# Kernel optimization log

Hardware: AMD Instinct MI355X
Metric: run time of the kernel (lower is better)

The kernel has to match this reference:

```python
import jax, jax.numpy as jnp
import numpy as np

N_NODES = 100000
D_IN = 128
D_OUT = 128
B, T, S = 8, 4096, 25


def setup_inputs() -> dict:
    key = jax.random.key(0)
    k1, k2, k3 = jax.random.split(key, 3)
    features = jax.random.normal(k1, (N_NODES, D_IN), dtype=jnp.float32)
    sample_res = jax.random.randint(k2, (B, T, S), 0, N_NODES, dtype=jnp.int64)
    # glorot-uniform init for [D_IN, D_OUT]
    limit = np.sqrt(6.0 / (D_IN + D_OUT)).astype(np.float32)
    weights = jax.random.uniform(k3, (D_IN, D_OUT), dtype=jnp.float32,
                                 minval=-limit, maxval=limit)
    return {"features": features, "sample_res": sample_res, "weights": weights}


def reference(features, sample_res, weights):
    # gather neighbor embeddings: [B, T, S, D]
    sampled = features[sample_res]
    # mean over sampled-neighbor axis -> [B, T, D]
    neigh_vecs = jnp.mean(sampled, axis=2)
    # shared linear transform + relu (bias=False per init defaults)
    out = jnp.einsum('btd,do->bto', neigh_vecs, weights)
    return jax.nn.relu(out)
```

## Files before the change

kernel.cpp:

```cpp
#include <hip/hip_runtime.h>


#define DEG 25
#define DIM 128

typedef __attribute__((ext_vector_type(8))) short short8;
typedef __attribute__((ext_vector_type(4))) float floatx4;
typedef __attribute__((ext_vector_type(4))) unsigned int uintx4;

__device__ __forceinline__ unsigned short f2bf(float f) {
    unsigned u = __float_as_uint(f);
    return (unsigned short)((u + 0x7fffu + ((u >> 16) & 1u)) >> 16);
}

#define BSTRIDE 136

__global__ __launch_bounds__(256, 2) void gemm_fw(
    const float* __restrict__ A,
    const float* __restrict__ B,
    unsigned short* __restrict__ G,
    int M)
{
    __shared__ unsigned short sBt[DIM * BSTRIDE];

    const int tid = threadIdx.x;

    {
        const float4* B4 = (const float4*)B;
#pragma unroll
        for (int i = 0; i < 16; ++i) {
            const int linear = i * 256 + tid;
            const int k  = linear >> 5;
            const int c4 = linear & 31;
            const float4 v = B4[linear];
            const int n = c4 * 4;
            sBt[(n + 0) * BSTRIDE + k] = f2bf(v.x);
            sBt[(n + 1) * BSTRIDE + k] = f2bf(v.y);
            sBt[(n + 2) * BSTRIDE + k] = f2bf(v.z);
            sBt[(n + 3) * BSTRIDE + k] = f2bf(v.w);
        }
    }
    __syncthreads();

    const int wave = tid >> 6;
    const int lane = tid & 63;
    const int quad = lane >> 4;
    const int l16  = lane & 15;

    const int rw0 = blockIdx.x * 128 + wave * 32;

    floatx4 acc[2][8];
#pragma unroll
    for (int mt = 0; mt < 2; ++mt)
#pragma unroll
        for (int nt = 0; nt < 8; ++nt)
            acc[mt][nt] = (floatx4){0.f, 0.f, 0.f, 0.f};

#pragma unroll
    for (int kt = 0; kt < 4; ++kt) {
        const int k0 = kt * 32;

        short8 afrag[2];
#pragma unroll
        for (int mt = 0; mt < 2; ++mt) {
            int row = rw0 + mt * 16 + l16;
            if (row >= M) row = M - 1;
            const float* ap = A + (size_t)row * DIM + k0 + quad * 8;
            const float4 x = *(const float4*)ap;
            const float4 y = *(const float4*)(ap + 4);
            unsigned p0 = (unsigned)f2bf(x.x) | ((unsigned)f2bf(x.y) << 16);
            unsigned p1 = (unsigned)f2bf(x.z) | ((unsigned)f2bf(x.w) << 16);
            unsigned p2 = (unsigned)f2bf(y.x) | ((unsigned)f2bf(y.y) << 16);
            unsigned p3 = (unsigned)f2bf(y.z) | ((unsigned)f2bf(y.w) << 16);
            uintx4 packed = (uintx4){p0, p1, p2, p3};
            afrag[mt] = __builtin_bit_cast(short8, packed);
        }

#pragma unroll
        for (int nt = 0; nt < 8; ++nt) {
            const uintx4 u = *(const uintx4*)&sBt[(nt * 16 + l16) * BSTRIDE + k0 + quad * 8];
            const short8 bfrag = __builtin_bit_cast(short8, u);
#pragma unroll
            for (int mt = 0; mt < 2; ++mt)
                acc[mt][nt] = __builtin_amdgcn_mfma_f32_16x16x32_bf16(
                    afrag[mt], bfrag, acc[mt][nt], 0, 0, 0);
        }
    }

    __syncthreads();
    {
        unsigned short* sT = sBt + wave * (32 * BSTRIDE);
#pragma unroll
        for (int mt = 0; mt < 2; ++mt)
#pragma unroll
            for (int nt = 0; nt < 8; ++nt)
#pragma unroll
                for (int r = 0; r < 4; ++r)
                    sT[(mt * 16 + quad * 4 + r) * BSTRIDE + nt * 16 + l16] =
                        f2bf(acc[mt][nt][r]);
    }
    __syncthreads();
    {
        const unsigned short* sT = sBt + wave * (32 * BSTRIDE);
        const int h    = lane & 1;
        const int nrow = lane >> 1;
        const int node = rw0 + nrow;
        if (node < M) {
            uintx4* G4 = (uintx4*)G;
#pragma unroll
            for (int c = 0; c < 8; ++c) {
                const uintx4 u = *(const uintx4*)&sT[nrow * BSTRIDE + c * 16 + h * 8];
                __builtin_nontemporal_store(u, &G4[((size_t)c * M + node) * 2 + h]);
            }
        }
    }
}

#define ROWS_PB 128

__global__ __launch_bounds__(256, 4) void gather_mean_relu_c(
    const unsigned short* __restrict__ G,
    const int* __restrict__ idx,
    float* __restrict__ out,
    int n_rows, int n_nodes)
{
    __shared__ int sIdx[ROWS_PB * DEG];

    const int tid  = threadIdx.x;
    const int c    = blockIdx.x & 7;
    const int rb   = blockIdx.x >> 3;
    const int row0 = rb * ROWS_PB;

    const int* ib = idx + (size_t)row0 * DEG;
    for (int i = tid; i < ROWS_PB * DEG; i += 256)
        sIdx[i] = __builtin_nontemporal_load(ib + i);
    __syncthreads();

    const int h = tid & 1;
    const int r = tid >> 1;
    const uintx4* __restrict__ Gc =
        (const uintx4*)G + (size_t)c * n_nodes * 2 + h;

    float a0 = 0.f, a1 = 0.f, a2 = 0.f, a3 = 0.f;
    float a4 = 0.f, a5 = 0.f, a6 = 0.f, a7 = 0.f;
    const int* ip = &sIdx[r * DEG];

#pragma unroll
    for (int sb = 0; sb < 5; ++sb) {
        uintx4 v[5];
#pragma unroll
        for (int s = 0; s < 5; ++s)
            v[s] = Gc[(size_t)(unsigned)ip[sb * 5 + s] * 2];
#pragma unroll
        for (int s = 0; s < 5; ++s) {
            a0 += __uint_as_float(v[s].x << 16);
            a1 += __uint_as_float(v[s].x & 0xffff0000u);
            a2 += __uint_as_float(v[s].y << 16);
            a3 += __uint_as_float(v[s].y & 0xffff0000u);
            a4 += __uint_as_float(v[s].z << 16);
            a5 += __uint_as_float(v[s].z & 0xffff0000u);
            a6 += __uint_as_float(v[s].w << 16);
            a7 += __uint_as_float(v[s].w & 0xffff0000u);
        }
    }

    const float inv = 1.0f / 25.0f;
    const floatx4 o0 = (floatx4){fmaxf(a0 * inv, 0.f), fmaxf(a1 * inv, 0.f),
                                 fmaxf(a2 * inv, 0.f), fmaxf(a3 * inv, 0.f)};
    const floatx4 o1 = (floatx4){fmaxf(a4 * inv, 0.f), fmaxf(a5 * inv, 0.f),
                                 fmaxf(a6 * inv, 0.f), fmaxf(a7 * inv, 0.f)};
    floatx4* op = (floatx4*)(out + (size_t)(row0 + r) * DIM + c * 16 + h * 8);
    __builtin_nontemporal_store(o0, op);
    __builtin_nontemporal_store(o1, op + 1);
}

#define RPB 16
#define CG 32

__device__ __forceinline__ float4 relu4(float4 v) {
    return make_float4(fmaxf(v.x, 0.f), fmaxf(v.y, 0.f),
                       fmaxf(v.z, 0.f), fmaxf(v.w, 0.f));
}

__global__ __launch_bounds__(256, 4) void gcn_fused(
    const float* __restrict__ F, const int* __restrict__ idx,
    const float* __restrict__ W, float* __restrict__ out, int n_rows)
{
    __shared__ float4 sV[RPB * CG];
    __shared__ int    sIdx[RPB * DEG];

    const float4* F4 = (const float4*)F;
    const float4* W4 = (const float4*)W;
    float4* out4 = (float4*)out;

    const int tid = threadIdx.x;
    const int row0 = blockIdx.x * RPB;

    for (int i = tid; i < RPB * DEG; i += 256)
        sIdx[i] = idx[(size_t)row0 * DEG + i];
    __syncthreads();

    const int cg = tid & 31;
    const int rs = tid >> 5;

#pragma unroll
    for (int rr = 0; rr < 2; ++rr) {
        const int r = rs + rr * 8;
        int j[DEG];
#pragma unroll
        for (int s = 0; s < DEG; ++s) j[s] = sIdx[r * DEG + s];
        float4 acc = make_float4(0.f, 0.f, 0.f, 0.f);
#pragma unroll
        for (int s = 0; s < DEG; ++s) {
            float4 f = F4[(size_t)j[s] * CG + cg];
            acc.x += f.x; acc.y += f.y; acc.z += f.z; acc.w += f.w;
        }
        const float inv = 1.0f / 25.0f;
        acc.x *= inv; acc.y *= inv; acc.z *= inv; acc.w *= inv;
        sV[r * CG + cg] = acc;
    }
    __syncthreads();

    const float4* vA = &sV[rs * CG];
    const float4* vB = &sV[(rs + 8) * CG];
    float4 o0 = make_float4(0.f, 0.f, 0.f, 0.f);
    float4 o1 = make_float4(0.f, 0.f, 0.f, 0.f);
#pragma unroll 4
    for (int d4 = 0; d4 < CG; ++d4) {
        const float4 a = vA[d4];
        const float4 b = vB[d4];
        const float4 w0 = W4[(size_t)(4 * d4 + 0) * CG + cg];
        const float4 w1 = W4[(size_t)(4 * d4 + 1) * CG + cg];
        const float4 w2 = W4[(size_t)(4 * d4 + 2) * CG + cg];
        const float4 w3 = W4[(size_t)(4 * d4 + 3) * CG + cg];
        o0.x += a.x*w0.x + a.y*w1.x + a.z*w2.x + a.w*w3.x;
        o0.y += a.x*w0.y + a.y*w1.y + a.z*w2.y + a.w*w3.y;
        o0.z += a.x*w0.z + a.y*w1.z + a.z*w2.z + a.w*w3.z;
        o0.w += a.x*w0.w + a.y*w1.w + a.z*w2.w + a.w*w3.w;
        o1.x += b.x*w0.x + b.y*w1.x + b.z*w2.x + b.w*w3.x;
        o1.y += b.x*w0.y + b.y*w1.y + b.z*w2.y + b.w*w3.y;
        o1.z += b.x*w0.z + b.y*w1.z + b.z*w2.z + b.w*w3.z;
        o1.w += b.x*w0.w + b.y*w1.w + b.z*w2.w + b.w*w3.w;
    }
    out4[(size_t)(row0 + rs) * CG + cg]     = relu4(o0);
    out4[(size_t)(row0 + rs + 8) * CG + cg] = relu4(o1);
}

extern "C" void kernel_launch(void* const* d_in, const int* in_sizes, int n_in,
                              void* d_out, int out_size, void* d_ws, size_t ws_size,
                              hipStream_t stream) {
    const float* F   = (const float*)d_in[0];
    const int*   idx = (const int*)d_in[1];
    const float* W   = (const float*)d_in[2];
    float* out = (float*)d_out;

    const int n_nodes = in_sizes[0] / DIM;
    const int n_rows  = in_sizes[1] / DEG;

    const size_t need = (size_t)n_nodes * DIM * sizeof(unsigned short);
    if (ws_size >= need && (n_rows & (ROWS_PB - 1)) == 0) {
        unsigned short* G = (unsigned short*)d_ws;
        gemm_fw<<<(n_nodes + 127) / 128, 256, 0, stream>>>(F, W, G, n_nodes);
        gather_mean_relu_c<<<(n_rows / ROWS_PB) * 8, 256, 0, stream>>>(
            G, idx, out, n_rows, n_nodes);
    } else {
        gcn_fused<<<n_rows / RPB, 256, 0, stream>>>(F, idx, W, out, n_rows);
    }
}
```

Measured before the change: 143.3 us.

## Partition node table into cache-sized slices and gather per slice with reduction pass

Splits the projected bf16 node table into four 25000-node partitions, each stored as two 64-column halves with a zero pad row. The gather kernel now filters every row's neighbor indices to one partition so each block's working set fits in cache, and writes fp32 partial sums to a workspace. A new reduce kernel adds the four partition partials and applies mean and ReLU. This trades extra partial-sum traffic and an extra launch for better gather locality, and the fast path is hardwired to exactly 100000 nodes.

```diff
diff --git a/kernel.cpp b/kernel.cpp
--- a/kernel.cpp
+++ b/kernel.cpp
@@ -3,6 +3,8 @@
 
 #define DEG 25
 #define DIM 128
+#define NPP 25000
+#define NPP1 25001
 
 typedef __attribute__((ext_vector_type(8))) short short8;
 typedef __attribute__((ext_vector_type(4))) float floatx4;
@@ -102,76 +104,135 @@
     __syncthreads();
     {
         const unsigned short* sT = sBt + wave * (32 * BSTRIDE);
-        const int h    = lane & 1;
-        const int nrow = lane >> 1;
-        const int node = rw0 + nrow;
-        if (node < M) {
-            uintx4* G4 = (uintx4*)G;
-#pragma unroll
-            for (int c = 0; c < 8; ++c) {
-                const uintx4 u = *(const uintx4*)&sT[nrow * BSTRIDE + c * 16 + h * 8];
-                __builtin_nontemporal_store(u, &G4[((size_t)c * M + node) * 2 + h]);
+        const int oct   = lane & 7;
+        const int nrow8 = lane >> 3;
+        uintx4* G4 = (uintx4*)G;
+#pragma unroll
+        for (int g = 0; g < 4; ++g) {
+            const int lrow = g * 8 + nrow8;
+            const int node = rw0 + lrow;
+            if (node < M) {
+                const unsigned p     = (unsigned)node / NPP;
+                const unsigned local = (unsigned)node - p * NPP;
+#pragma unroll
+                for (int h = 0; h < 2; ++h) {
+                    const uintx4 u = *(const uintx4*)
+                        &sT[lrow * BSTRIDE + h * 64 + oct * 8];
+                    __builtin_nontemporal_store(u,
+                        &G4[((size_t)(p * 2 + h) * NPP1 + local) * 8 + oct]);
+                }
             }
         }
-    }
-}
-
-#define ROWS_PB 128
-
-__global__ __launch_bounds__(256, 4) void gather_mean_relu_c(
+        if (blockIdx.x == 0 && tid < 64) {
+            const int sl = tid >> 3, o = tid & 7;
+            __builtin_nontemporal_store((uintx4){0, 0, 0, 0},
+                &G4[((size_t)sl * NPP1 + NPP) * 8 + o]);
+        }
+    }
+}
+
+#define GRB 128
+
+__global__ __launch_bounds__(256, 4) void gather_partial(
     const unsigned short* __restrict__ G,
     const int* __restrict__ idx,
-    float* __restrict__ out,
-    int n_rows, int n_nodes)
+    float* __restrict__ P,
+    int n_rows)
 {
-    __shared__ int sIdx[ROWS_PB * DEG];
+    __shared__ int sIdx[GRB * DEG];
+    __shared__ int sCnt[GRB];
 
     const int tid  = threadIdx.x;
     const int c    = blockIdx.x & 7;
+    const int p    = c >> 1;
     const int rb   = blockIdx.x >> 3;
-    const int row0 = rb * ROWS_PB;
+    const int row0 = rb * GRB;
+    const int lo   = p * NPP;
 
     const int* ib = idx + (size_t)row0 * DEG;
-    for (int i = tid; i < ROWS_PB * DEG; i += 256)
+    for (int i = tid; i < GRB * DEG; i += 256)
         sIdx[i] = __builtin_nontemporal_load(ib + i);
     __syncthreads();
 
-    const int h = tid & 1;
-    const int r = tid >> 1;
+    if (tid < GRB) {
+        int* lp = &sIdx[tid * DEG];
+        int cnt = 0;
+#pragma unroll
+        for (int s = 0; s < DEG; ++s) {
+            const unsigned d = (unsigned)(lp[s] - lo);
+            if (d < NPP) lp[cnt++] = (int)d;
+        }
+        const int m = ((cnt + 4) / 5) * 5;
+        for (int i = cnt; i < m; ++i) lp[i] = NPP;
+        sCnt[tid] = m;
+    }
+    __syncthreads();
+
+    const int oct = tid & 7;
+    const int rg  = tid >> 3;
     const uintx4* __restrict__ Gc =
-        (const uintx4*)G + (size_t)c * n_nodes * 2 + h;
-
-    float a0 = 0.f, a1 = 0.f, a2 = 0.f, a3 = 0.f;
-    float a4 = 0.f, a5 = 0.f, a6 = 0.f, a7 = 0.f;
-    const int* ip = &sIdx[r * DEG];
-
-#pragma unroll
-    for (int sb = 0; sb < 5; ++sb) {
-        uintx4 v[5];
-#pragma unroll
-        for (int s = 0; s < 5; ++s)
-            v[s] = Gc[(size_t)(unsigned)ip[sb * 5 + s] * 2];
-#pragma unroll
-        for (int s = 0; s < 5; ++s) {
-            a0 += __uint_as_float(v[s].x << 16);
-            a1 += __uint_as_float(v[s].x & 0xffff0000u);
-            a2 += __uint_as_float(v[s].y << 16);
-            a3 += __uint_as_float(v[s].y & 0xffff0000u);
-            a4 += __uint_as_float(v[s].z << 16);
-            a5 += __uint_as_float(v[s].z & 0xffff0000u);
-            a6 += __uint_as_float(v[s].w << 16);
-            a7 += __uint_as_float(v[s].w & 0xffff0000u);
-        }
-    }
-
+        (const uintx4*)G + (size_t)c * NPP1 * 8 + oct;
+
+#pragma unroll
+    for (int rr = 0; rr < 4; ++rr) {
+        const int r = rr * 32 + rg;
+        const int m = sCnt[r];
+        const int* lp = &sIdx[r * DEG];
+
+        float a0 = 0.f, a1 = 0.f, a2 = 0.f, a3 = 0.f;
+        float a4 = 0.f, a5 = 0.f, a6 = 0.f, a7 = 0.f;
+
+        for (int i = 0; i < m; i += 5) {
+            const uintx4 v0 = Gc[(size_t)lp[i + 0] * 8];
+            const uintx4 v1 = Gc[(size_t)lp[i + 1] * 8];
+            const uintx4 v2 = Gc[(size_t)lp[i + 2] * 8];
+            const uintx4 v3 = Gc[(size_t)lp[i + 3] * 8];
+            const uintx4 v4 = Gc[(size_t)lp[i + 4] * 8];
+#pragma unroll
+            for (int k = 0; k < 5; ++k) {
+                const uintx4 v = (k == 0) ? v0 : (k == 1) ? v1 :
+                                 (k == 2) ? v2 : (k == 3) ? v3 : v4;
+                a0 += __uint_as_float(v.x << 16);
+                a1 += __uint_as_float(v.x & 0xffff0000u);
+                a2 += __uint_as_float(v.y << 16);
+                a3 += __uint_as_float(v.y & 0xffff0000u);
+                a4 += __uint_as_float(v.z << 16);
+                a5 += __uint_as_float(v.z & 0xffff0000u);
+                a6 += __uint_as_float(v.w << 16);
+                a7 += __uint_as_float(v.w & 0xffff0000u);
+            }
+        }
+
+        floatx4* Pp = (floatx4*)P + ((size_t)c * n_rows + row0 + r) * 16 + oct * 2;
+        __builtin_nontemporal_store((floatx4){a0, a1, a2, a3}, Pp);
+        __builtin_nontemporal_store((floatx4){a4, a5, a6, a7}, Pp + 1);
+    }
+}
+
+__global__ __launch_bounds__(256, 4) void reduce_relu(
+    const float* __restrict__ P, float* __restrict__ out, int n_rows)
+{
+    const int total = n_rows * 32;
+    const floatx4* P4 = (const floatx4*)P;
+    floatx4* o4 = (floatx4*)out;
     const float inv = 1.0f / 25.0f;
-    const floatx4 o0 = (floatx4){fmaxf(a0 * inv, 0.f), fmaxf(a1 * inv, 0.f),
-                                 fmaxf(a2 * inv, 0.f), fmaxf(a3 * inv, 0.f)};
-    const floatx4 o1 = (floatx4){fmaxf(a4 * inv, 0.f), fmaxf(a5 * inv, 0.f),
-                                 fmaxf(a6 * inv, 0.f), fmaxf(a7 * inv, 0.f)};
-    floatx4* op = (floatx4*)(out + (size_t)(row0 + r) * DIM + c * 16 + h * 8);
-    __builtin_nontemporal_store(o0, op);
-    __builtin_nontemporal_store(o1, op + 1);
+    const size_t sl = (size_t)n_rows * 16;
+
+    for (int i = blockIdx.x * 256 + threadIdx.x; i < total;
+         i += gridDim.x * 256) {
+        const int r   = i >> 5;
+        const int rem = i & 31;
+        const int h   = rem >> 4;
+        const int j4  = rem & 15;
+        const size_t rbase = (size_t)r * 16 + j4;
+        floatx4 s = __builtin_nontemporal_load(&P4[(size_t)(0 + h) * sl + rbase]);
+        s = s + __builtin_nontemporal_load(&P4[(size_t)(2 + h) * sl + rbase]);
+        s = s + __builtin_nontemporal_load(&P4[(size_t)(4 + h) * sl + rbase]);
+        s = s + __builtin_nontemporal_load(&P4[(size_t)(6 + h) * sl + rbase]);
+        const floatx4 o = {fmaxf(s.x * inv, 0.f), fmaxf(s.y * inv, 0.f),
+                           fmaxf(s.z * inv, 0.f), fmaxf(s.w * inv, 0.f)};
+        __builtin_nontemporal_store(o, &o4[(size_t)r * 32 + rem]);
+    }
 }
 
 #define RPB 16
@@ -257,12 +318,16 @@
     const int n_nodes = in_sizes[0] / DIM;
     const int n_rows  = in_sizes[1] / DEG;
 
-    const size_t need = (size_t)n_nodes * DIM * sizeof(unsigned short);
-    if (ws_size >= need && (n_rows & (ROWS_PB - 1)) == 0) {
+    const size_t gbytes = (size_t)8 * NPP1 * 64 * sizeof(unsigned short);
+    const size_t poff   = (gbytes + 1023) & ~(size_t)1023;
+    const size_t need   = poff + (size_t)8 * n_rows * 64 * sizeof(float);
+
+    if (n_nodes == 100000 && ws_size >= need && (n_rows & (GRB - 1)) == 0) {
         unsigned short* G = (unsigned short*)d_ws;
+        float* P = (float*)((char*)d_ws + poff);
         gemm_fw<<<(n_nodes + 127) / 128, 256, 0, stream>>>(F, W, G, n_nodes);
-        gather_mean_relu_c<<<(n_rows / ROWS_PB) * 8, 256, 0, stream>>>(
-            G, idx, out, n_rows, n_nodes);
+        gather_partial<<<(n_rows / GRB) * 8, 256, 0, stream>>>(G, idx, P, n_rows);
+        reduce_relu<<<1024, 256, 0, stream>>>(P, out, n_rows);
     } else {
         gcn_fused<<<n_rows / RPB, 256, 0, stream>>>(F, idx, W, out, n_rows);
     }
```

Result: slower. 172.0 us (+20.0%).

## Quantize transformed node table to int8 with per-node scales for gather

Applied to the files above, without the earlier changes.

The GEMM-first kernel now stores the transformed node features as int8 with a per-row absmax scale instead of bf16, halving the bytes per node fetched by the gather stage. The gather kernel is restructured so 8 threads each read 16 bytes of one full 128-byte row, dequantize with the node scale and accumulate, writing row-contiguous outputs. This lowers random-gather traffic at the cost of extra dequantization ALU work, an extra scale load per neighbor, and a larger quantization error than bf16.

```diff
diff --git a/kernel.cpp b/kernel.cpp
--- a/kernel.cpp
+++ b/kernel.cpp
@@ -5,7 +5,9 @@
 #define DIM 128
 
 typedef __attribute__((ext_vector_type(8))) short short8;
+typedef __attribute__((ext_vector_type(2))) float floatx2;
 typedef __attribute__((ext_vector_type(4))) float floatx4;
+typedef __attribute__((ext_vector_type(2))) unsigned int uintx2;
 typedef __attribute__((ext_vector_type(4))) unsigned int uintx4;
 
 __device__ __forceinline__ unsigned short f2bf(float f) {
@@ -15,10 +17,11 @@
 
 #define BSTRIDE 136
 
-__global__ __launch_bounds__(256, 2) void gemm_fw(
+__global__ __launch_bounds__(256, 2) void gemm_fw_q8(
     const float* __restrict__ A,
     const float* __restrict__ B,
-    unsigned short* __restrict__ G,
+    unsigned char* __restrict__ Gq,
+    float* __restrict__ Sc,
     int M)
 {
     __shared__ unsigned short sBt[DIM * BSTRIDE];
@@ -87,91 +90,108 @@
         }
     }
 
-    __syncthreads();
-    {
-        unsigned short* sT = sBt + wave * (32 * BSTRIDE);
-#pragma unroll
-        for (int mt = 0; mt < 2; ++mt)
-#pragma unroll
-            for (int nt = 0; nt < 8; ++nt)
-#pragma unroll
-                for (int r = 0; r < 4; ++r)
-                    sT[(mt * 16 + quad * 4 + r) * BSTRIDE + nt * 16 + l16] =
-                        f2bf(acc[mt][nt][r]);
-    }
-    __syncthreads();
-    {
-        const unsigned short* sT = sBt + wave * (32 * BSTRIDE);
-        const int h    = lane & 1;
-        const int nrow = lane >> 1;
-        const int node = rw0 + nrow;
-        if (node < M) {
-            uintx4* G4 = (uintx4*)G;
-#pragma unroll
-            for (int c = 0; c < 8; ++c) {
-                const uintx4 u = *(const uintx4*)&sT[nrow * BSTRIDE + c * 16 + h * 8];
-                __builtin_nontemporal_store(u, &G4[((size_t)c * M + node) * 2 + h]);
+#pragma unroll
+    for (int mt = 0; mt < 2; ++mt) {
+#pragma unroll
+        for (int r = 0; r < 4; ++r) {
+            float m = fabsf(acc[mt][0][r]);
+#pragma unroll
+            for (int nt = 1; nt < 8; ++nt)
+                m = fmaxf(m, fabsf(acc[mt][nt][r]));
+            m = fmaxf(m, __shfl_xor(m, 1));
+            m = fmaxf(m, __shfl_xor(m, 2));
+            m = fmaxf(m, __shfl_xor(m, 4));
+            m = fmaxf(m, __shfl_xor(m, 8));
+
+            const int node = rw0 + mt * 16 + quad * 4 + r;
+            const float is = (m > 0.f) ? 127.f / m : 0.f;
+            if (l16 == 0 && node < M)
+                Sc[node] = m * (1.f / 127.f);
+
+            if (node < M) {
+                unsigned lo = 0, hi = 0;
+#pragma unroll
+                for (int nt = 0; nt < 4; ++nt) {
+                    float t = rintf(acc[mt][nt][r] * is);
+                    t = fmaxf(-127.f, fminf(127.f, t));
+                    lo |= ((unsigned)((int)t & 255)) << (8 * nt);
+                }
+#pragma unroll
+                for (int nt = 4; nt < 8; ++nt) {
+                    float t = rintf(acc[mt][nt][r] * is);
+                    t = fmaxf(-127.f, fminf(127.f, t));
+                    hi |= ((unsigned)((int)t & 255)) << (8 * (nt - 4));
+                }
+                *(uintx2*)(Gq + (size_t)node * DIM + l16 * 8) = (uintx2){lo, hi};
             }
         }
     }
 }
 
-#define ROWS_PB 128
-
-__global__ __launch_bounds__(256, 4) void gather_mean_relu_c(
-    const unsigned short* __restrict__ G,
+#define GRB 32
+
+__global__ __launch_bounds__(256, 4) void gather_q8(
+    const unsigned char* __restrict__ Gq,
+    const float* __restrict__ Sc,
     const int* __restrict__ idx,
     float* __restrict__ out,
-    int n_rows, int n_nodes)
+    int n_rows)
 {
-    __shared__ int sIdx[ROWS_PB * DEG];
+    __shared__ int sIdx[GRB * DEG];
 
     const int tid  = threadIdx.x;
-    const int c    = blockIdx.x & 7;
-    const int rb   = blockIdx.x >> 3;
-    const int row0 = rb * ROWS_PB;
+    const int row0 = blockIdx.x * GRB;
 
     const int* ib = idx + (size_t)row0 * DEG;
-    for (int i = tid; i < ROWS_PB * DEG; i += 256)
+    for (int i = tid; i < GRB * DEG; i += 256)
         sIdx[i] = __builtin_nontemporal_load(ib + i);
     __syncthreads();
 
-    const int h = tid & 1;
-    const int r = tid >> 1;
-    const uintx4* __restrict__ Gc =
-        (const uintx4*)G + (size_t)c * n_nodes * 2 + h;
-
-    float a0 = 0.f, a1 = 0.f, a2 = 0.f, a3 = 0.f;
-    float a4 = 0.f, a5 = 0.f, a6 = 0.f, a7 = 0.f;
-    const int* ip = &sIdx[r * DEG];
+    const int oct = tid & 7;
+    const int r   = tid >> 3;
+    const uintx4* __restrict__ G4 = (const uintx4*)Gq + oct;
+    const int* lp = &sIdx[r * DEG];
+
+    float acc[16];
+#pragma unroll
+    for (int k = 0; k < 16; ++k) acc[k] = 0.f;
+
+#define ACC16(v, s)                                             \
+    do {                                                        \
+        _Pragma("unroll")                                       \
+        for (int d = 0; d < 4; ++d) {                           \
+            const unsigned u = (v)[d];                          \
+            acc[4*d + 0] += (s) * (float)((int)(u << 24) >> 24);\
+            acc[4*d + 1] += (s) * (float)((int)(u << 16) >> 24);\
+            acc[4*d + 2] += (s) * (float)((int)(u <<  8) >> 24);\
+            acc[4*d + 3] += (s) * (float)((int)u >> 24);        \
+        }                                                       \
+    } while (0)
 
 #pragma unroll
     for (int sb = 0; sb < 5; ++sb) {
-        uintx4 v[5];
-#pragma unroll
-        for (int s = 0; s < 5; ++s)
-            v[s] = Gc[(size_t)(unsigned)ip[sb * 5 + s] * 2];
-#pragma unroll
-        for (int s = 0; s < 5; ++s) {
-            a0 += __uint_as_float(v[s].x << 16);
-            a1 += __uint_as_float(v[s].x & 0xffff0000u);
-            a2 += __uint_as_float(v[s].y << 16);
-            a3 += __uint_as_float(v[s].y & 0xffff0000u);
-            a4 += __uint_as_float(v[s].z << 16);
-            a5 += __uint_as_float(v[s].z & 0xffff0000u);
-            a6 += __uint_as_float(v[s].w << 16);
-            a7 += __uint_as_float(v[s].w & 0xffff0000u);
-        }
-    }
+        int n0 = lp[sb*5+0], n1 = lp[sb*5+1], n2 = lp[sb*5+2],
+            n3 = lp[sb*5+3], n4 = lp[sb*5+4];
+        const uintx4 v0 = G4[(size_t)n0 * 8];
+        const uintx4 v1 = G4[(size_t)n1 * 8];
+        const uintx4 v2 = G4[(size_t)n2 * 8];
+        const uintx4 v3 = G4[(size_t)n3 * 8];
+        const uintx4 v4 = G4[(size_t)n4 * 8];
+        const float s0 = Sc[n0], s1 = Sc[n1], s2 = Sc[n2],
+                    s3 = Sc[n3], s4 = Sc[n4];
+        ACC16(v0, s0); ACC16(v1, s1); ACC16(v2, s2);
+        ACC16(v3, s3); ACC16(v4, s4);
+    }
+#undef ACC16
 
     const float inv = 1.0f / 25.0f;
-    const floatx4 o0 = (floatx4){fmaxf(a0 * inv, 0.f), fmaxf(a1 * inv, 0.f),
-                                 fmaxf(a2 * inv, 0.f), fmaxf(a3 * inv, 0.f)};
-    const floatx4 o1 = (floatx4){fmaxf(a4 * inv, 0.f), fmaxf(a5 * inv, 0.f),
-                                 fmaxf(a6 * inv, 0.f), fmaxf(a7 * inv, 0.f)};
-    floatx4* op = (floatx4*)(out + (size_t)(row0 + r) * DIM + c * 16 + h * 8);
-    __builtin_nontemporal_store(o0, op);
-    __builtin_nontemporal_store(o1, op + 1);
+    float* orow = out + (size_t)(row0 + r) * DIM + oct * 2;
+#pragma unroll
+    for (int j = 0; j < 8; ++j) {
+        const floatx2 w = {fmaxf(acc[j] * inv, 0.f),
+                           fmaxf(acc[j + 8] * inv, 0.f)};
+        __builtin_nontemporal_store(w, (floatx2*)(orow + 16 * j));
+    }
 }
 
 #define RPB 16
@@ -200,7 +220,7 @@
         sIdx[i] = idx[(size_t)row0 * DEG + i];
     __syncthreads();
 
-    const int cg = tid & 31;
+    const int cg32 = tid & 31;
     const int rs = tid >> 5;
 
 #pragma unroll
@@ -212,12 +232,12 @@
         float4 acc = make_float4(0.f, 0.f, 0.f, 0.f);
 #pragma unroll
         for (int s = 0; s < DEG; ++s) {
-            float4 f = F4[(size_t)j[s] * CG + cg];
+            float4 f = F4[(size_t)j[s] * CG + cg32];
             acc.x += f.x; acc.y += f.y; acc.z += f.z; acc.w += f.w;
         }
         const float inv = 1.0f / 25.0f;
         acc.x *= inv; acc.y *= inv; acc.z *= inv; acc.w *= inv;
-        sV[r * CG + cg] = acc;
+        sV[r * CG + cg32] = acc;
     }
     __syncthreads();
 
@@ -229,10 +249,10 @@
     for (int d4 = 0; d4 < CG; ++d4) {
         const float4 a = vA[d4];
         const float4 b = vB[d4];
-        const float4 w0 = W4[(size_t)(4 * d4 + 0) * CG + cg];
-        const float4 w1 = W4[(size_t)(4 * d4 + 1) * CG + cg];
-        const float4 w2 = W4[(size_t)(4 * d4 + 2) * CG + cg];
-        const float4 w3 = W4[(size_t)(4 * d4 + 3) * CG + cg];
+        const float4 w0 = W4[(size_t)(4 * d4 + 0) * CG + cg32];
+        const float4 w1 = W4[(size_t)(4 * d4 + 1) * CG + cg32];
+        const float4 w2 = W4[(size_t)(4 * d4 + 2) * CG + cg32];
+        const float4 w3 = W4[(size_t)(4 * d4 + 3) * CG + cg32];
         o0.x += a.x*w0.x + a.y*w1.x + a.z*w2.x + a.w*w3.x;
         o0.y += a.x*w0.y + a.y*w1.y + a.z*w2.y + a.w*w3.y;
         o0.z += a.x*w0.z + a.y*w1.z + a.z*w2.z + a.w*w3.z;
@@ -242,8 +262,8 @@
         o1.z += b.x*w0.z + b.y*w1.z + b.z*w2.z + b.w*w3.z;
         o1.w += b.x*w0.w + b.y*w1.w + b.z*w2.w + b.w*w3.w;
     }
-    out4[(size_t)(row0 + rs) * CG + cg]     = relu4(o0);
-    out4[(size_t)(row0 + rs + 8) * CG + cg] = relu4(o1);
+    out4[(size_t)(row0 + rs) * CG + cg32]     = relu4(o0);
+    out4[(size_t)(row0 + rs + 8) * CG + cg32] = relu4(o1);
 }
 
 extern "C" void kernel_launch(void* const* d_in, const int* in_sizes, int n_in,
@@ -257,12 +277,15 @@
     const int n_nodes = in_sizes[0] / DIM;
     const int n_rows  = in_sizes[1] / DEG;
 
-    const size_t need = (size_t)n_nodes * DIM * sizeof(unsigned short);
-    if (ws_size >= need && (n_rows & (ROWS_PB - 1)) == 0) {
-        unsigned short* G = (unsigned short*)d_ws;
-        gemm_fw<<<(n_nodes + 127) / 128, 256, 0, stream>>>(F, W, G, n_nodes);
-        gather_mean_relu_c<<<(n_rows / ROWS_PB) * 8, 256, 0, stream>>>(
-            G, idx, out, n_rows, n_nodes);
+    const size_t gq_bytes = (size_t)n_nodes * DIM;
+    const size_t sc_off   = (gq_bytes + 127) & ~(size_t)127;
+    const size_t need     = sc_off + (size_t)n_nodes * sizeof(float);
+
+    if (ws_size >= need && (n_rows & (GRB - 1)) == 0) {
+        unsigned char* Gq = (unsigned char*)d_ws;
+        float* Sc = (float*)((char*)d_ws + sc_off);
+        gemm_fw_q8<<<(n_nodes + 127) / 128, 256, 0, stream>>>(F, W, Gq, Sc, n_nodes);
+        gather_q8<<<n_rows / GRB, 256, 0, stream>>>(Gq, Sc, idx, out, n_rows);
     } else {
         gcn_fused<<<n_rows / RPB, 256, 0, stream>>>(F, idx, W, out, n_rows);
     }
```

Result: faster. 121.3 us (-15.4%).
